# Optimization experiments

Hardware: AMD Instinct MI355X
Metric: run time of the kernel (lower is better)

The kernel has to match this reference:

```python
import jax, jax.numpy as jnp
import numpy as np

B, S, H, C = 8, 4096, 768, 64  # batch, seq_len, hidden_dim, block size


def _xavier(k, shape):
    fan = shape[0] + shape[1]
    return jax.random.normal(k, shape, jnp.float32) * np.sqrt(2.0 / fan)


def setup_inputs() -> dict:
    key = jax.random.key(0)
    kx, kq, kk, kv, k1, k2 = jax.random.split(key, 6)
    return {
        "x": jax.random.normal(kx, (B, S, H), jnp.float32),
        "Wq": _xavier(kq, (H, H)),
        "Wk": _xavier(kk, (H, H)),
        "Wv": _xavier(kv, (H, H)),
        "W1": _xavier(k1, (H, 16)),
        "W2": _xavier(k2, (16, H)),
        "b": jnp.zeros((H,), jnp.float32),
    }


def reference(x, Wq, Wk, Wv, W1, W2, b):
    Bb, Ss, Hh = x.shape
    NB = Ss // C  # number of blocks (seq_len divisible by C, no remainder)
    Q = x @ Wq
    K = x @ Wk
    V = x @ Wv
    # gating alpha: identical every block iteration in the original, compute once
    alpha = jax.nn.sigmoid((x @ W1) @ W2 + b) ** (1.0 / 16.0)  # [B,S,H]
    a = alpha.mean(axis=1, keepdims=True)  # [B,1,H], broadcasts over rows of state
    # blocks to leading axis for scan: [NB, B, C, H]
    qs = Q.reshape(Bb, NB, C, Hh).transpose(1, 0, 2, 3)
    ks = K.reshape(Bb, NB, C, Hh).transpose(1, 0, 2, 3)
    vs = V.reshape(Bb, NB, C, Hh).transpose(1, 0, 2, 3)
    mask = jnp.tril(jnp.ones((C, C), x.dtype))
    scale = 1.0 / np.sqrt(Hh).astype(np.float32)

    def step(St, blk):
        qb, kb, vb = blk  # each [B,C,H]
        # state update first (original updates S before computing output)
        St = St * a + jnp.einsum("bch,bcd->bhd", kb, vb)  # [B,H,H]
        # intra-block: scores masked by MULTIPLICATION (as in original), then softmax
        scores = jnp.einsum("bch,bdh->bcd", qb, kb) * mask * scale
        w = jax.nn.softmax(scores, axis=-1)
        out = jnp.einsum("bch,bhd->bcd", qb, St) + jnp.einsum("bcd,bde->bce", w, vb)
        return St, out

    S0 = jnp.zeros((Bb, Hh, Hh), x.dtype)
    _, outs = jax.lax.scan(step, S0, (qs, ks, vs))  # outs: [NB,B,C,H]
    O = outs.transpose(1, 0, 2, 3).reshape(Bb, Ss, Hh)
    return O
```

## Files before the change

kernel.cpp:

```cpp
#include <hip/hip_runtime.h>

#define B_ 8
#define S_ 4096
#define H_ 768
#define C_ 64
#define NB_ 64
#define M_ (B_*S_)

typedef _Float16 f16x8 __attribute__((ext_vector_type(8)));
typedef _Float16 f16x4 __attribute__((ext_vector_type(4)));
typedef float    f32x4 __attribute__((ext_vector_type(4)));

__global__ __launch_bounds__(256) void k_transpose(const float* __restrict__ src,
                                                   _Float16* __restrict__ dst) {
  __shared__ float tile[32][33];
  const int t = threadIdx.x;
  const int tx = t & 31, ty = t >> 5;
  const int n0 = blockIdx.x * 32, k0 = blockIdx.y * 32;
#pragma unroll
  for (int i = 0; i < 4; ++i)
    tile[ty + i*8][tx] = src[(k0 + ty + i*8) * H_ + n0 + tx];
  __syncthreads();
#pragma unroll
  for (int i = 0; i < 4; ++i)
    dst[(n0 + ty + i*8) * H_ + k0 + tx] = (_Float16)tile[tx][ty + i*8];
}

__global__ __launch_bounds__(256) void k_gemm_qkv(
    const float* __restrict__ x,
    const _Float16* __restrict__ WqT, const _Float16* __restrict__ WkT,
    const _Float16* __restrict__ WvT,
    _Float16* __restrict__ Qb, _Float16* __restrict__ Vb,
    _Float16* __restrict__ KT, _Float16* __restrict__ VT) {
  __shared__ _Float16 xs[64][40];
  __shared__ _Float16 ws[3][128][40];
  const int t = threadIdx.x;
  const int m0 = blockIdx.x * 64, n0 = blockIdx.y * 128;
  const int lane = t & 63, wv = t >> 6;
  const int lm = lane & 15, qd = lane >> 4;
  const int sm = t >> 2, sk = (t & 3) * 8;
  const int wn = t >> 1, wk = (t & 1) * 16;

  f32x4 acc[3][4][2];
#pragma unroll
  for (int a = 0; a < 3; ++a)
#pragma unroll
    for (int i = 0; i < 4; ++i)
#pragma unroll
      for (int n = 0; n < 2; ++n)
        acc[a][i][n] = (f32x4){0.f, 0.f, 0.f, 0.f};

  for (int kk = 0; kk < 24; ++kk) {
    const int k0 = kk * 32;
    __syncthreads();
    {
      const f32x4* xp = (const f32x4*)&x[(size_t)(m0 + sm) * H_ + k0 + sk];
      f32x4 f0 = xp[0], f1 = xp[1];
      f16x8 xv;
#pragma unroll
      for (int j = 0; j < 4; ++j) { xv[j] = (_Float16)f0[j]; xv[4 + j] = (_Float16)f1[j]; }
      *(f16x8*)&xs[sm][sk] = xv;
    }
    {
      const f16x8* wp = (const f16x8*)&WqT[(n0 + wn) * H_ + k0 + wk];
      *(f16x8*)&ws[0][wn][wk] = wp[0]; *(f16x8*)&ws[0][wn][wk + 8] = wp[1];
      wp = (const f16x8*)&WkT[(n0 + wn) * H_ + k0 + wk];
      *(f16x8*)&ws[1][wn][wk] = wp[0]; *(f16x8*)&ws[1][wn][wk + 8] = wp[1];
      wp = (const f16x8*)&WvT[(n0 + wn) * H_ + k0 + wk];
      *(f16x8*)&ws[2][wn][wk] = wp[0]; *(f16x8*)&ws[2][wn][wk + 8] = wp[1];
    }
    __syncthreads();
    f16x8 af[4];
#pragma unroll
    for (int i = 0; i < 4; ++i) af[i] = *(f16x8*)&xs[i*16 + lm][qd*8];
#pragma unroll
    for (int a = 0; a < 3; ++a)
#pragma unroll
      for (int n = 0; n < 2; ++n) {
        f16x8 bfr = *(f16x8*)&ws[a][wv*32 + n*16 + lm][qd*8];
#pragma unroll
        for (int i = 0; i < 4; ++i)
          acc[a][i][n] = __builtin_amdgcn_mfma_f32_16x16x32_f16(af[i], bfr, acc[a][i][n], 0, 0, 0);
      }
  }
#pragma unroll
  for (int i = 0; i < 4; ++i)
#pragma unroll
    for (int n = 0; n < 2; ++n) {
      const int ng = n0 + wv*32 + n*16 + lm;
      const int mg0 = m0 + i*16 + qd*4;
      const int bb = mg0 >> 12, ss = mg0 & (S_ - 1);
#pragma unroll
      for (int r = 0; r < 4; ++r) {
        Qb[(size_t)(mg0 + r) * H_ + ng] = (_Float16)acc[0][i][n][r];
        Vb[(size_t)(mg0 + r) * H_ + ng] = (_Float16)acc[2][i][n][r];
      }
      f16x4 kp, vp;
#pragma unroll
      for (int r = 0; r < 4; ++r) {
        kp[r] = (_Float16)acc[1][i][n][r];
        vp[r] = (_Float16)acc[2][i][n][r];
      }
      *(f16x4*)&KT[((size_t)bb * H_ + ng) * S_ + ss] = kp;
      *(f16x4*)&VT[((size_t)bb * H_ + ng) * S_ + ss] = vp;
    }
}

__global__ __launch_bounds__(256) void k_tgemm(const float* __restrict__ x,
                                               const float* __restrict__ W1,
                                               float* __restrict__ tbuf) {
  __shared__ float w1s[768 * 16];
  __shared__ float xs[64 * 129];
  const int t = threadIdx.x;
  const int m0 = blockIdx.x * 64;
  for (int i = t; i < 768 * 16 / 4; i += 256)
    ((f32x4*)w1s)[i] = ((const f32x4*)W1)[i];
  const int row = t & 63, cg = t >> 6;
  f32x4 acc = (f32x4){0.f, 0.f, 0.f, 0.f};
  for (int kc = 0; kc < 768; kc += 128) {
    __syncthreads();
    for (int i = 0; i < 32; ++i) {
      const int idx = t + 256 * i;
      const int r = idx >> 7, c = idx & 127;
      xs[r * 129 + c] = x[(size_t)(m0 + r) * H_ + kc + c];
    }
    __syncthreads();
#pragma unroll 8
    for (int kl = 0; kl < 128; ++kl) {
      const float a = xs[row * 129 + kl];
      const f32x4 w = *(const f32x4*)&w1s[(kc + kl) * 16 + cg * 4];
#pragma unroll
      for (int j = 0; j < 4; ++j) acc[j] += a * w[j];
    }
  }
  *(f32x4*)&tbuf[(size_t)(m0 + row) * 16 + cg * 4] = acc;
}

__global__ __launch_bounds__(256) void k_areduce(const float* __restrict__ tbuf,
                                                 const float* __restrict__ W2,
                                                 const float* __restrict__ bias,
                                                 float* __restrict__ abuf) {
  __shared__ float ts[128 * 17];
  __shared__ float rbuf[8 * 32];
  const int t = threadIdx.x;
  const int b = blockIdx.y, hc = blockIdx.x;
  const int hl = t & 31, sg = t >> 5;
  const int h = hc * 32 + hl;
  float w2r[16];
#pragma unroll
  for (int j = 0; j < 16; ++j) w2r[j] = W2[j * H_ + h];
  const float bb = bias[h];
  float asum = 0.f;
  const float* tb = &tbuf[(size_t)(b * S_) * 16];
  for (int sc = 0; sc < S_; sc += 128) {
    __syncthreads();
    for (int i = 0; i < 8; ++i) {
      const int idx = t + 256 * i;
      const int sl = idx >> 4, j = idx & 15;
      ts[sl * 17 + j] = tb[(size_t)(sc + sl) * 16 + j];
    }
    __syncthreads();
    for (int i = 0; i < 16; ++i) {
      const int sl = sg + i * 8;
      float z = bb;
      const float* tr = &ts[sl * 17];
#pragma unroll
      for (int j = 0; j < 16; ++j) z += tr[j] * w2r[j];
      const float sgm = 1.f / (1.f + __expf(-z));
      asum += sqrtf(sqrtf(sqrtf(sqrtf(sgm))));
    }
  }
  rbuf[sg * 32 + hl] = asum;
  __syncthreads();
  if (t < 32) {
    float s = 0.f;
#pragma unroll
    for (int g = 0; g < 8; ++g) s += rbuf[g * 32 + t];
    abuf[b * H_ + hc * 32 + t] = s * (1.f / (float)S_);
  }
}

__global__ __launch_bounds__(256) void k_scores_y(
    const _Float16* __restrict__ Qb, const _Float16* __restrict__ KT,
    const _Float16* __restrict__ Vb, float* __restrict__ O) {
  __shared__ float qs[64 * 68];
  __shared__ float ks[64 * 68];
  __shared__ float wb[64 * 68];
  __shared__ float vsb[64 * 68];
  const int t = threadIdx.x;
  const int nb = blockIdx.x, b = blockIdx.y;
  const size_t base = ((size_t)b * S_ + nb * 64) * H_;
  const int tc = t >> 4, td = t & 15;
  const int srow = t >> 2, sseg = (t & 3) * 16;

  float scr[4][4];
#pragma unroll
  for (int i = 0; i < 4; ++i)
#pragma unroll
    for (int u = 0; u < 4; ++u) scr[i][u] = 0.f;

  for (int hc = 0; hc < 12; ++hc) {
    __syncthreads();
    {
      const f16x8* qp = (const f16x8*)&Qb[base + (size_t)srow * H_ + hc * 64 + sseg];
      f16x8 q0 = qp[0], q1 = qp[1];
#pragma unroll
      for (int j = 0; j < 8; ++j) {
        qs[(sseg + j) * 68 + srow] = (float)q0[j];
        qs[(sseg + 8 + j) * 68 + srow] = (float)q1[j];
      }
    }
    {
      const size_t krow = ((size_t)b * H_ + hc * 64 + srow) * S_ + nb * 64 + sseg;
      f16x8 k0 = *(const f16x8*)&KT[krow];
      f16x8 k1 = *(const f16x8*)&KT[krow + 8];
      f32x4 f;
#pragma unroll
      for (int j = 0; j < 4; ++j) f[j] = (float)k0[j];
      *(f32x4*)&ks[srow * 68 + sseg] = f;
#pragma unroll
      for (int j = 0; j < 4; ++j) f[j] = (float)k0[4 + j];
      *(f32x4*)&ks[srow * 68 + sseg + 4] = f;
#pragma unroll
      for (int j = 0; j < 4; ++j) f[j] = (float)k1[j];
      *(f32x4*)&ks[srow * 68 + sseg + 8] = f;
#pragma unroll
      for (int j = 0; j < 4; ++j) f[j] = (float)k1[4 + j];
      *(f32x4*)&ks[srow * 68 + sseg + 12] = f;
    }
    __syncthreads();
#pragma unroll 4
    for (int h = 0; h < 64; ++h) {
      const f32x4 qv = *(f32x4*)&qs[h * 68 + tc * 4];
      const f32x4 kv = *(f32x4*)&ks[h * 68 + td * 4];
#pragma unroll
      for (int i = 0; i < 4; ++i)
#pragma unroll
        for (int u = 0; u < 4; ++u) scr[i][u] += qv[i] * kv[u];
    }
  }
  const float scale = 0.036084391824351615f;
#pragma unroll
  for (int i = 0; i < 4; ++i)
#pragma unroll
    for (int u = 0; u < 4; ++u) {
      const int c = tc * 4 + i, d = td * 4 + u;
      wb[d * 68 + c] = (d <= c) ? scr[i][u] * scale : 0.f;
    }
  __syncthreads();
  {
    const int r = t >> 2, g = t & 3;
    float vals[16];
    float mx = -1e30f;
#pragma unroll
    for (int i = 0; i < 16; ++i) {
      vals[i] = wb[(g * 16 + i) * 68 + r];
      mx = fmaxf(mx, vals[i]);
    }
    mx = fmaxf(mx, __shfl_xor(mx, 1));
    mx = fmaxf(mx, __shfl_xor(mx, 2));
    float sm = 0.f;
#pragma unroll
    for (int i = 0; i < 16; ++i) { vals[i] = __expf(vals[i] - mx); sm += vals[i]; }
    sm += __shfl_xor(sm, 1);
    sm += __shfl_xor(sm, 2);
    const float inv = 1.f / sm;
#pragma unroll
    for (int i = 0; i < 16; ++i) wb[(g * 16 + i) * 68 + r] = vals[i] * inv;
  }
  for (int ec = 0; ec < 12; ++ec) {
    __syncthreads();
    {
      const f16x8* vp = (const f16x8*)&Vb[base + (size_t)srow * H_ + ec * 64 + sseg];
      f16x8 v0 = vp[0], v1 = vp[1];
      f32x4 f;
#pragma unroll
      for (int j = 0; j < 4; ++j) f[j] = (float)v0[j];
      *(f32x4*)&vsb[srow * 68 + sseg] = f;
#pragma unroll
      for (int j = 0; j < 4; ++j) f[j] = (float)v0[4 + j];
      *(f32x4*)&vsb[srow * 68 + sseg + 4] = f;
#pragma unroll
      for (int j = 0; j < 4; ++j) f[j] = (float)v1[j];
      *(f32x4*)&vsb[srow * 68 + sseg + 8] = f;
#pragma unroll
      for (int j = 0; j < 4; ++j) f[j] = (float)v1[4 + j];
      *(f32x4*)&vsb[srow * 68 + sseg + 12] = f;
    }
    __syncthreads();
    float y[4][4];
#pragma unroll
    for (int i = 0; i < 4; ++i)
#pragma unroll
      for (int u = 0; u < 4; ++u) y[i][u] = 0.f;
#pragma unroll 4
    for (int j = 0; j < 64; ++j) {
      const f32x4 wv = *(f32x4*)&wb[j * 68 + tc * 4];
      const f32x4 vv = *(f32x4*)&vsb[j * 68 + td * 4];
#pragma unroll
      for (int i = 0; i < 4; ++i)
#pragma unroll
        for (int u = 0; u < 4; ++u) y[i][u] += wv[i] * vv[u];
    }
#pragma unroll
    for (int i = 0; i < 4; ++i) {
      f32x4 yv = {y[i][0], y[i][1], y[i][2], y[i][3]};
      *(f32x4*)&O[base + (size_t)(tc * 4 + i) * H_ + ec * 64 + td * 4] = yv;
    }
  }
}

#define STP 776
__global__ __launch_bounds__(256, 2) void k_scan(
    const _Float16* __restrict__ Qb, const _Float16* __restrict__ KT,
    const _Float16* __restrict__ VT, const float* __restrict__ abuf,
    float* __restrict__ O) {
  __shared__ _Float16 StL[32 * STP];
  const int t = threadIdx.x;
  const int b = blockIdx.y;
  const int d0 = blockIdx.x * 32;
  const int w = t >> 6, lane = t & 63;
  const int lm = lane & 15, qd = lane >> 4;

  const float av0 = abuf[b * H_ + d0 + lm];
  const float av1 = abuf[b * H_ + d0 + 16 + lm];

  f32x4 acc[12][2];
#pragma unroll
  for (int mt = 0; mt < 12; ++mt) {
    acc[mt][0] = (f32x4){0.f, 0.f, 0.f, 0.f};
    acc[mt][1] = (f32x4){0.f, 0.f, 0.f, 0.f};
  }

  const size_t ktb = (size_t)b * H_ * S_;
  const size_t vrow0 = ktb + (size_t)(d0 + lm) * S_;
  const size_t vrow1 = ktb + (size_t)(d0 + 16 + lm) * S_;

  for (int blk = 0; blk < NB_; ++blk) {
    const int s0 = blk * 64;
    f16x8 vf00 = *(const f16x8*)&VT[vrow0 + s0 + qd * 8];
    f16x8 vf01 = *(const f16x8*)&VT[vrow0 + s0 + 32 + qd * 8];
    f16x8 vf10 = *(const f16x8*)&VT[vrow1 + s0 + qd * 8];
    f16x8 vf11 = *(const f16x8*)&VT[vrow1 + s0 + 32 + qd * 8];
#pragma unroll
    for (int mt = 0; mt < 12; ++mt) {
      const size_t arow = ktb + (size_t)((w * 12 + mt) * 16 + lm) * S_ + s0 + qd * 8;
      f16x8 a0 = *(const f16x8*)&KT[arow];
      f16x8 a1 = *(const f16x8*)&KT[arow + 32];
      f32x4 c0 = acc[mt][0] * av0;
      f32x4 c1 = acc[mt][1] * av1;
      c0 = __builtin_amdgcn_mfma_f32_16x16x32_f16(a0, vf00, c0, 0, 0, 0);
      c0 = __builtin_amdgcn_mfma_f32_16x16x32_f16(a1, vf01, c0, 0, 0, 0);
      c1 = __builtin_amdgcn_mfma_f32_16x16x32_f16(a0, vf10, c1, 0, 0, 0);
      c1 = __builtin_amdgcn_mfma_f32_16x16x32_f16(a1, vf11, c1, 0, 0, 0);
      acc[mt][0] = c0;
      acc[mt][1] = c1;
    }
    __syncthreads();
#pragma unroll
    for (int mt = 0; mt < 12; ++mt) {
      const int h = (w * 12 + mt) * 16 + qd * 4;
      f16x4 p0, p1;
#pragma unroll
      for (int r = 0; r < 4; ++r) {
        p0[r] = (_Float16)acc[mt][0][r];
        p1[r] = (_Float16)acc[mt][1][r];
      }
      *(f16x4*)&StL[lm * STP + h] = p0;
      *(f16x4*)&StL[(16 + lm) * STP + h] = p1;
    }
    __syncthreads();
    f32x4 o0a = {0.f,0.f,0.f,0.f}, o0b = {0.f,0.f,0.f,0.f};
    f32x4 o1a = {0.f,0.f,0.f,0.f}, o1b = {0.f,0.f,0.f,0.f};
    const size_t qrow = ((size_t)b * S_ + s0 + w * 16 + lm) * H_ + qd * 8;
#pragma unroll 3
    for (int kt = 0; kt < 24; kt += 2) {
      f16x8 qa = *(const f16x8*)&Qb[qrow + kt * 32];
      f16x8 qb2 = *(const f16x8*)&Qb[qrow + kt * 32 + 32];
      f16x8 s00 = *(f16x8*)&StL[lm * STP + kt * 32 + qd * 8];
      f16x8 s01 = *(f16x8*)&StL[(16 + lm) * STP + kt * 32 + qd * 8];
      f16x8 s10 = *(f16x8*)&StL[lm * STP + kt * 32 + 32 + qd * 8];
      f16x8 s11 = *(f16x8*)&StL[(16 + lm) * STP + kt * 32 + 32 + qd * 8];
      o0a = __builtin_amdgcn_mfma_f32_16x16x32_f16(qa, s00, o0a, 0, 0, 0);
      o1a = __builtin_amdgcn_mfma_f32_16x16x32_f16(qa, s01, o1a, 0, 0, 0);
      o0b = __builtin_amdgcn_mfma_f32_16x16x32_f16(qb2, s10, o0b, 0, 0, 0);
      o1b = __builtin_amdgcn_mfma_f32_16x16x32_f16(qb2, s11, o1b, 0, 0, 0);
    }
    const f32x4 o0 = o0a + o0b;
    const f32x4 o1 = o1a + o1b;
    const size_t orow = ((size_t)b * S_ + s0 + w * 16 + qd * 4) * H_ + d0;
#pragma unroll
    for (int r = 0; r < 4; ++r) {
      O[orow + (size_t)r * H_ + lm] += o0[r];
      O[orow + (size_t)r * H_ + 16 + lm] += o1[r];
    }
  }
}

extern "C" void kernel_launch(void* const* d_in, const int* in_sizes, int n_in,
                              void* d_out, int out_size, void* d_ws, size_t ws_size,
                              hipStream_t stream) {
  (void)in_sizes; (void)n_in; (void)out_size; (void)ws_size;
  const float* x    = (const float*)d_in[0];
  const float* Wq   = (const float*)d_in[1];
  const float* Wk   = (const float*)d_in[2];
  const float* Wv   = (const float*)d_in[3];
  const float* W1   = (const float*)d_in[4];
  const float* W2   = (const float*)d_in[5];
  const float* bias = (const float*)d_in[6];
  float* O = (float*)d_out;

  char* ws = (char*)d_ws;
  _Float16* Qb  = (_Float16*)ws;
  _Float16* Vb  = Qb + (size_t)M_ * H_;
  _Float16* KT  = Vb + (size_t)M_ * H_;
  _Float16* VT  = KT + (size_t)M_ * H_;
  _Float16* WqT = VT + (size_t)M_ * H_;
  _Float16* WkT = WqT + H_ * H_;
  _Float16* WvT = WkT + H_ * H_;
  float* tbuf = (float*)(WvT + H_ * H_);
  float* abuf = tbuf + (size_t)M_ * 16;

  k_transpose<<<dim3(24, 24), 256, 0, stream>>>(Wq, WqT);
  k_transpose<<<dim3(24, 24), 256, 0, stream>>>(Wk, WkT);
  k_transpose<<<dim3(24, 24), 256, 0, stream>>>(Wv, WvT);
  k_gemm_qkv<<<dim3(512, 6), 256, 0, stream>>>(x, WqT, WkT, WvT, Qb, Vb, KT, VT);
  k_tgemm<<<dim3(512), 256, 0, stream>>>(x, W1, tbuf);
  k_areduce<<<dim3(24, 8), 256, 0, stream>>>(tbuf, W2, bias, abuf);
  k_scores_y<<<dim3(64, 8), 256, 0, stream>>>(Qb, KT, Vb, O);
  k_scan<<<dim3(24, 8), 256, 0, stream>>>(Qb, KT, VT, abuf, O);
}
```

Baseline: 1.536 ms.

## Split scan over hidden chunks with partial outputs, MFMA intra-block scores, prefetch K/V

The intra-block scores and softmax-weighted V product move from scalar fp32 LDS loops to MFMA fp16 instructions that read the transposed K and V buffers, so the row-major V buffer is dropped. The sequential scan kernel is split along the hidden (contraction) dimension into 2 or 4 chunks, picked by available workspace. This multiplies the number of blocks in the latency-bound scan, and K/V fragments for the next block are prefetched through register double-buffering. Each chunk writes fp16 partial outputs that a new reduce kernel adds into O. The cost is extra memory traffic for the partials and lower precision in the partial sums.

Result: slower. 1.876 ms (+22.1%).

```diff
diff --git a/kernel.cpp b/kernel.cpp
--- a/kernel.cpp
+++ b/kernel.cpp
@@ -30,8 +30,7 @@
     const float* __restrict__ x,
     const _Float16* __restrict__ WqT, const _Float16* __restrict__ WkT,
     const _Float16* __restrict__ WvT,
-    _Float16* __restrict__ Qb, _Float16* __restrict__ Vb,
-    _Float16* __restrict__ KT, _Float16* __restrict__ VT) {
+    _Float16* __restrict__ Qb, _Float16* __restrict__ KT, _Float16* __restrict__ VT) {
   __shared__ _Float16 xs[64][40];
   __shared__ _Float16 ws[3][128][40];
   const int t = threadIdx.x;
@@ -91,10 +90,8 @@
       const int mg0 = m0 + i*16 + qd*4;
       const int bb = mg0 >> 12, ss = mg0 & (S_ - 1);
 #pragma unroll
-      for (int r = 0; r < 4; ++r) {
+      for (int r = 0; r < 4; ++r)
         Qb[(size_t)(mg0 + r) * H_ + ng] = (_Float16)acc[0][i][n][r];
-        Vb[(size_t)(mg0 + r) * H_ + ng] = (_Float16)acc[2][i][n][r];
-      }
       f16x4 kp, vp;
 #pragma unroll
       for (int r = 0; r < 4; ++r) {
@@ -182,225 +179,224 @@
 
 __global__ __launch_bounds__(256) void k_scores_y(
     const _Float16* __restrict__ Qb, const _Float16* __restrict__ KT,
-    const _Float16* __restrict__ Vb, float* __restrict__ O) {
-  __shared__ float qs[64 * 68];
-  __shared__ float ks[64 * 68];
-  __shared__ float wb[64 * 68];
-  __shared__ float vsb[64 * 68];
+    const _Float16* __restrict__ VT, float* __restrict__ O) {
+  __shared__ _Float16 sbuf[64 * 136];
   const int t = threadIdx.x;
   const int nb = blockIdx.x, b = blockIdx.y;
-  const size_t base = ((size_t)b * S_ + nb * 64) * H_;
-  const int tc = t >> 4, td = t & 15;
-  const int srow = t >> 2, sseg = (t & 3) * 16;
-
-  float scr[4][4];
-#pragma unroll
-  for (int i = 0; i < 4; ++i)
-#pragma unroll
-    for (int u = 0; u < 4; ++u) scr[i][u] = 0.f;
-
-  for (int hc = 0; hc < 12; ++hc) {
+  const int s0 = nb * 64;
+  const int w = t >> 6, lane = t & 63;
+  const int lm = lane & 15, qd = lane >> 4;
+
+  f32x4 sc[4];
+#pragma unroll
+  for (int nt = 0; nt < 4; ++nt) sc[nt] = (f32x4){0.f, 0.f, 0.f, 0.f};
+
+  for (int hr = 0; hr < 6; ++hr) {
     __syncthreads();
     {
-      const f16x8* qp = (const f16x8*)&Qb[base + (size_t)srow * H_ + hc * 64 + sseg];
-      f16x8 q0 = qp[0], q1 = qp[1];
-#pragma unroll
-      for (int j = 0; j < 8; ++j) {
-        qs[(sseg + j) * 68 + srow] = (float)q0[j];
-        qs[(sseg + 8 + j) * 68 + srow] = (float)q1[j];
-      }
-    }
-    {
-      const size_t krow = ((size_t)b * H_ + hc * 64 + srow) * S_ + nb * 64 + sseg;
-      f16x8 k0 = *(const f16x8*)&KT[krow];
-      f16x8 k1 = *(const f16x8*)&KT[krow + 8];
-      f32x4 f;
-#pragma unroll
-      for (int j = 0; j < 4; ++j) f[j] = (float)k0[j];
-      *(f32x4*)&ks[srow * 68 + sseg] = f;
-#pragma unroll
-      for (int j = 0; j < 4; ++j) f[j] = (float)k0[4 + j];
-      *(f32x4*)&ks[srow * 68 + sseg + 4] = f;
-#pragma unroll
-      for (int j = 0; j < 4; ++j) f[j] = (float)k1[j];
-      *(f32x4*)&ks[srow * 68 + sseg + 8] = f;
-#pragma unroll
-      for (int j = 0; j < 4; ++j) f[j] = (float)k1[4 + j];
-      *(f32x4*)&ks[srow * 68 + sseg + 12] = f;
-    }
-    __syncthreads();
-#pragma unroll 4
-    for (int h = 0; h < 64; ++h) {
-      const f32x4 qv = *(f32x4*)&qs[h * 68 + tc * 4];
-      const f32x4 kv = *(f32x4*)&ks[h * 68 + td * 4];
-#pragma unroll
-      for (int i = 0; i < 4; ++i)
-#pragma unroll
-        for (int u = 0; u < 4; ++u) scr[i][u] += qv[i] * kv[u];
-    }
-  }
+      const int hl = t >> 1, dseg = (t & 1) * 32;
+      const size_t krow = ((size_t)b * H_ + hr * 128 + hl) * S_ + s0 + dseg;
+#pragma unroll
+      for (int j = 0; j < 4; ++j) {
+        f16x8 kv = *(const f16x8*)&KT[krow + j * 8];
+#pragma unroll
+        for (int u = 0; u < 8; ++u) sbuf[(dseg + j * 8 + u) * 136 + hl] = kv[u];
+      }
+    }
+    __syncthreads();
+    const size_t qrow = ((size_t)b * S_ + s0 + w * 16 + lm) * H_ + hr * 128 + qd * 8;
+#pragma unroll
+    for (int ktl = 0; ktl < 4; ++ktl) {
+      f16x8 qa = *(const f16x8*)&Qb[qrow + ktl * 32];
+#pragma unroll
+      for (int nt = 0; nt < 4; ++nt) {
+        f16x8 kb = *(f16x8*)&sbuf[(nt * 16 + lm) * 136 + ktl * 32 + qd * 8];
+        sc[nt] = __builtin_amdgcn_mfma_f32_16x16x32_f16(qa, kb, sc[nt], 0, 0, 0);
+      }
+    }
+  }
+  __syncthreads();
   const float scale = 0.036084391824351615f;
 #pragma unroll
-  for (int i = 0; i < 4; ++i)
-#pragma unroll
-    for (int u = 0; u < 4; ++u) {
-      const int c = tc * 4 + i, d = td * 4 + u;
-      wb[d * 68 + c] = (d <= c) ? scr[i][u] * scale : 0.f;
-    }
-  __syncthreads();
-  {
-    const int r = t >> 2, g = t & 3;
-    float vals[16];
-    float mx = -1e30f;
-#pragma unroll
-    for (int i = 0; i < 16; ++i) {
-      vals[i] = wb[(g * 16 + i) * 68 + r];
-      mx = fmaxf(mx, vals[i]);
+  for (int r = 0; r < 4; ++r) {
+    const int c = w * 16 + qd * 4 + r;
+    float v[4]; float mx = -1e30f;
+#pragma unroll
+    for (int nt = 0; nt < 4; ++nt) {
+      const int d = nt * 16 + lm;
+      v[nt] = (d <= c) ? sc[nt][r] * scale : 0.f;
+      mx = fmaxf(mx, v[nt]);
     }
     mx = fmaxf(mx, __shfl_xor(mx, 1));
     mx = fmaxf(mx, __shfl_xor(mx, 2));
+    mx = fmaxf(mx, __shfl_xor(mx, 4));
+    mx = fmaxf(mx, __shfl_xor(mx, 8));
     float sm = 0.f;
 #pragma unroll
-    for (int i = 0; i < 16; ++i) { vals[i] = __expf(vals[i] - mx); sm += vals[i]; }
+    for (int nt = 0; nt < 4; ++nt) { v[nt] = __expf(v[nt] - mx); sm += v[nt]; }
     sm += __shfl_xor(sm, 1);
     sm += __shfl_xor(sm, 2);
+    sm += __shfl_xor(sm, 4);
+    sm += __shfl_xor(sm, 8);
     const float inv = 1.f / sm;
 #pragma unroll
-    for (int i = 0; i < 16; ++i) wb[(g * 16 + i) * 68 + r] = vals[i] * inv;
-  }
-  for (int ec = 0; ec < 12; ++ec) {
-    __syncthreads();
-    {
-      const f16x8* vp = (const f16x8*)&Vb[base + (size_t)srow * H_ + ec * 64 + sseg];
-      f16x8 v0 = vp[0], v1 = vp[1];
-      f32x4 f;
-#pragma unroll
-      for (int j = 0; j < 4; ++j) f[j] = (float)v0[j];
-      *(f32x4*)&vsb[srow * 68 + sseg] = f;
-#pragma unroll
-      for (int j = 0; j < 4; ++j) f[j] = (float)v0[4 + j];
-      *(f32x4*)&vsb[srow * 68 + sseg + 4] = f;
-#pragma unroll
-      for (int j = 0; j < 4; ++j) f[j] = (float)v1[j];
-      *(f32x4*)&vsb[srow * 68 + sseg + 8] = f;
-#pragma unroll
-      for (int j = 0; j < 4; ++j) f[j] = (float)v1[4 + j];
-      *(f32x4*)&vsb[srow * 68 + sseg + 12] = f;
-    }
-    __syncthreads();
-    float y[4][4];
-#pragma unroll
-    for (int i = 0; i < 4; ++i)
-#pragma unroll
-      for (int u = 0; u < 4; ++u) y[i][u] = 0.f;
+    for (int nt = 0; nt < 4; ++nt)
+      sbuf[c * 72 + nt * 16 + lm] = (_Float16)(v[nt] * inv);
+  }
+  __syncthreads();
+  f16x8 wf[4][2];
+#pragma unroll
+  for (int nt = 0; nt < 4; ++nt)
+#pragma unroll
+    for (int kd = 0; kd < 2; ++kd)
+      wf[nt][kd] = *(f16x8*)&sbuf[(nt * 16 + lm) * 72 + kd * 32 + qd * 8];
 #pragma unroll 4
-    for (int j = 0; j < 64; ++j) {
-      const f32x4 wv = *(f32x4*)&wb[j * 68 + tc * 4];
-      const f32x4 vv = *(f32x4*)&vsb[j * 68 + td * 4];
-#pragma unroll
-      for (int i = 0; i < 4; ++i)
-#pragma unroll
-        for (int u = 0; u < 4; ++u) y[i][u] += wv[i] * vv[u];
-    }
-#pragma unroll
-    for (int i = 0; i < 4; ++i) {
-      f32x4 yv = {y[i][0], y[i][1], y[i][2], y[i][3]};
-      *(f32x4*)&O[base + (size_t)(tc * 4 + i) * H_ + ec * 64 + td * 4] = yv;
-    }
-  }
-}
-
-#define STP 776
-__global__ __launch_bounds__(256, 2) void k_scan(
+  for (int mt = 0; mt < 12; ++mt) {
+    const int e0 = (w * 12 + mt) * 16;
+    const size_t ar = ((size_t)b * H_ + e0 + lm) * S_ + s0 + qd * 8;
+    f16x8 a0 = *(const f16x8*)&VT[ar];
+    f16x8 a1 = *(const f16x8*)&VT[ar + 32];
+#pragma unroll
+    for (int nt = 0; nt < 4; ++nt) {
+      f32x4 y = (f32x4){0.f, 0.f, 0.f, 0.f};
+      y = __builtin_amdgcn_mfma_f32_16x16x32_f16(a0, wf[nt][0], y, 0, 0, 0);
+      y = __builtin_amdgcn_mfma_f32_16x16x32_f16(a1, wf[nt][1], y, 0, 0, 0);
+      *(f32x4*)&O[((size_t)b * S_ + s0 + nt * 16 + lm) * H_ + e0 + qd * 4] = y;
+    }
+  }
+}
+
+template<int HC>
+__global__ __launch_bounds__(256, (HC == 4 ? 3 : 2)) void k_scan(
     const _Float16* __restrict__ Qb, const _Float16* __restrict__ KT,
     const _Float16* __restrict__ VT, const float* __restrict__ abuf,
-    float* __restrict__ O) {
+    _Float16* __restrict__ P, size_t pstride) {
+  constexpr int HCH = H_ / HC;
+  constexpr int MT  = HCH / 64;
+  constexpr int KT2 = HCH / 32;
+  constexpr int STP = HCH + 8;
   __shared__ _Float16 StL[32 * STP];
   const int t = threadIdx.x;
-  const int b = blockIdx.y;
   const int d0 = blockIdx.x * 32;
+  const int hcb = blockIdx.y;
+  const int b = blockIdx.z;
   const int w = t >> 6, lane = t & 63;
   const int lm = lane & 15, qd = lane >> 4;
 
   const float av0 = abuf[b * H_ + d0 + lm];
   const float av1 = abuf[b * H_ + d0 + 16 + lm];
 
-  f32x4 acc[12][2];
-#pragma unroll
-  for (int mt = 0; mt < 12; ++mt) {
+  f32x4 acc[MT][2];
+#pragma unroll
+  for (int mt = 0; mt < MT; ++mt) {
     acc[mt][0] = (f32x4){0.f, 0.f, 0.f, 0.f};
     acc[mt][1] = (f32x4){0.f, 0.f, 0.f, 0.f};
   }
 
-  const size_t ktb = (size_t)b * H_ * S_;
-  const size_t vrow0 = ktb + (size_t)(d0 + lm) * S_;
-  const size_t vrow1 = ktb + (size_t)(d0 + 16 + lm) * S_;
-
+  const size_t ktbase = (size_t)b * H_;
+  const size_t krow = (ktbase + hcb * HCH + w * MT * 16 + lm) * S_ + qd * 8;
+  const size_t vrow0 = (ktbase + d0 + lm) * S_ + qd * 8;
+  const size_t vrow1 = (ktbase + d0 + 16 + lm) * S_ + qd * 8;
+
+  f16x8 kfb[2][MT][2];
+  f16x8 vfb[2][2][2];
+#pragma unroll
+  for (int mt = 0; mt < MT; ++mt) {
+    kfb[0][mt][0] = *(const f16x8*)&KT[krow + (size_t)mt * 16 * S_];
+    kfb[0][mt][1] = *(const f16x8*)&KT[krow + (size_t)mt * 16 * S_ + 32];
+  }
+  vfb[0][0][0] = *(const f16x8*)&VT[vrow0];
+  vfb[0][0][1] = *(const f16x8*)&VT[vrow0 + 32];
+  vfb[0][1][0] = *(const f16x8*)&VT[vrow1];
+  vfb[0][1][1] = *(const f16x8*)&VT[vrow1 + 32];
+
+  _Float16* Pp = P + (size_t)hcb * pstride;
+
+#pragma unroll 1
   for (int blk = 0; blk < NB_; ++blk) {
+    const int cur = blk & 1, nxt = cur ^ 1;
     const int s0 = blk * 64;
-    f16x8 vf00 = *(const f16x8*)&VT[vrow0 + s0 + qd * 8];
-    f16x8 vf01 = *(const f16x8*)&VT[vrow0 + s0 + 32 + qd * 8];
-    f16x8 vf10 = *(const f16x8*)&VT[vrow1 + s0 + qd * 8];
-    f16x8 vf11 = *(const f16x8*)&VT[vrow1 + s0 + 32 + qd * 8];
-#pragma unroll
-    for (int mt = 0; mt < 12; ++mt) {
-      const size_t arow = ktb + (size_t)((w * 12 + mt) * 16 + lm) * S_ + s0 + qd * 8;
-      f16x8 a0 = *(const f16x8*)&KT[arow];
-      f16x8 a1 = *(const f16x8*)&KT[arow + 32];
+    f16x8 qf[KT2];
+    const size_t qrow = ((size_t)b * S_ + s0 + w * 16 + lm) * H_ + hcb * HCH + qd * 8;
+#pragma unroll
+    for (int kt = 0; kt < KT2; ++kt) qf[kt] = *(const f16x8*)&Qb[qrow + kt * 32];
+#pragma unroll
+    for (int mt = 0; mt < MT; ++mt) {
       f32x4 c0 = acc[mt][0] * av0;
       f32x4 c1 = acc[mt][1] * av1;
-      c0 = __builtin_amdgcn_mfma_f32_16x16x32_f16(a0, vf00, c0, 0, 0, 0);
-      c0 = __builtin_amdgcn_mfma_f32_16x16x32_f16(a1, vf01, c0, 0, 0, 0);
-      c1 = __builtin_amdgcn_mfma_f32_16x16x32_f16(a0, vf10, c1, 0, 0, 0);
-      c1 = __builtin_amdgcn_mfma_f32_16x16x32_f16(a1, vf11, c1, 0, 0, 0);
+      c0 = __builtin_amdgcn_mfma_f32_16x16x32_f16(kfb[cur][mt][0], vfb[cur][0][0], c0, 0, 0, 0);
+      c0 = __builtin_amdgcn_mfma_f32_16x16x32_f16(kfb[cur][mt][1], vfb[cur][0][1], c0, 0, 0, 0);
+      c1 = __builtin_amdgcn_mfma_f32_16x16x32_f16(kfb[cur][mt][0], vfb[cur][1][0], c1, 0, 0, 0);
+      c1 = __builtin_amdgcn_mfma_f32_16x16x32_f16(kfb[cur][mt][1], vfb[cur][1][1], c1, 0, 0, 0);
       acc[mt][0] = c0;
       acc[mt][1] = c1;
     }
     __syncthreads();
 #pragma unroll
-    for (int mt = 0; mt < 12; ++mt) {
-      const int h = (w * 12 + mt) * 16 + qd * 4;
+    for (int mt = 0; mt < MT; ++mt) {
+      const int hl = (w * MT + mt) * 16 + qd * 4;
       f16x4 p0, p1;
 #pragma unroll
       for (int r = 0; r < 4; ++r) {
         p0[r] = (_Float16)acc[mt][0][r];
         p1[r] = (_Float16)acc[mt][1][r];
       }
-      *(f16x4*)&StL[lm * STP + h] = p0;
-      *(f16x4*)&StL[(16 + lm) * STP + h] = p1;
-    }
-    __syncthreads();
-    f32x4 o0a = {0.f,0.f,0.f,0.f}, o0b = {0.f,0.f,0.f,0.f};
-    f32x4 o1a = {0.f,0.f,0.f,0.f}, o1b = {0.f,0.f,0.f,0.f};
-    const size_t qrow = ((size_t)b * S_ + s0 + w * 16 + lm) * H_ + qd * 8;
-#pragma unroll 3
-    for (int kt = 0; kt < 24; kt += 2) {
-      f16x8 qa = *(const f16x8*)&Qb[qrow + kt * 32];
-      f16x8 qb2 = *(const f16x8*)&Qb[qrow + kt * 32 + 32];
-      f16x8 s00 = *(f16x8*)&StL[lm * STP + kt * 32 + qd * 8];
-      f16x8 s01 = *(f16x8*)&StL[(16 + lm) * STP + kt * 32 + qd * 8];
-      f16x8 s10 = *(f16x8*)&StL[lm * STP + kt * 32 + 32 + qd * 8];
-      f16x8 s11 = *(f16x8*)&StL[(16 + lm) * STP + kt * 32 + 32 + qd * 8];
-      o0a = __builtin_amdgcn_mfma_f32_16x16x32_f16(qa, s00, o0a, 0, 0, 0);
-      o1a = __builtin_amdgcn_mfma_f32_16x16x32_f16(qa, s01, o1a, 0, 0, 0);
-      o0b = __builtin_amdgcn_mfma_f32_16x16x32_f16(qb2, s10, o0b, 0, 0, 0);
-      o1b = __builtin_amdgcn_mfma_f32_16x16x32_f16(qb2, s11, o1b, 0, 0, 0);
-    }
-    const f32x4 o0 = o0a + o0b;
-    const f32x4 o1 = o1a + o1b;
-    const size_t orow = ((size_t)b * S_ + s0 + w * 16 + qd * 4) * H_ + d0;
-#pragma unroll
-    for (int r = 0; r < 4; ++r) {
-      O[orow + (size_t)r * H_ + lm] += o0[r];
-      O[orow + (size_t)r * H_ + 16 + lm] += o1[r];
-    }
+      *(f16x4*)&StL[lm * STP + hl] = p0;
+      *(f16x4*)&StL[(16 + lm) * STP + hl] = p1;
+    }
+    __syncthreads();
+    if (blk < NB_ - 1) {
+      const int s1 = s0 + 64;
+#pragma unroll
+      for (int mt = 0; mt < MT; ++mt) {
+        kfb[nxt][mt][0] = *(const f16x8*)&KT[krow + (size_t)mt * 16 * S_ + s1];
+        kfb[nxt][mt][1] = *(const f16x8*)&KT[krow + (size_t)mt * 16 * S_ + s1 + 32];
+      }
+      vfb[nxt][0][0] = *(const f16x8*)&VT[vrow0 + s1];
+      vfb[nxt][0][1] = *(const f16x8*)&VT[vrow0 + s1 + 32];
+      vfb[nxt][1][0] = *(const f16x8*)&VT[vrow1 + s1];
+      vfb[nxt][1][1] = *(const f16x8*)&VT[vrow1 + s1 + 32];
+    }
+    f32x4 o0 = (f32x4){0.f, 0.f, 0.f, 0.f};
+    f32x4 o1 = (f32x4){0.f, 0.f, 0.f, 0.f};
+#pragma unroll
+    for (int kt = 0; kt < KT2; ++kt) {
+      f16x8 a0 = *(f16x8*)&StL[lm * STP + kt * 32 + qd * 8];
+      f16x8 a1 = *(f16x8*)&StL[(16 + lm) * STP + kt * 32 + qd * 8];
+      o0 = __builtin_amdgcn_mfma_f32_16x16x32_f16(a0, qf[kt], o0, 0, 0, 0);
+      o1 = __builtin_amdgcn_mfma_f32_16x16x32_f16(a1, qf[kt], o1, 0, 0, 0);
+    }
+    const size_t prow = ((size_t)b * S_ + s0 + w * 16 + lm) * H_ + d0 + qd * 4;
+    f16x4 q0, q1;
+#pragma unroll
+    for (int r = 0; r < 4; ++r) { q0[r] = (_Float16)o0[r]; q1[r] = (_Float16)o1[r]; }
+    *(f16x4*)&Pp[prow] = q0;
+    *(f16x4*)&Pp[prow + 16] = q1;
+  }
+}
+
+template<int HC>
+__global__ __launch_bounds__(256) void k_reduce(const _Float16* __restrict__ P,
+                                                size_t pstride, float* __restrict__ O) {
+  const int total = M_ * H_ / 8;
+  for (int i = blockIdx.x * 256 + threadIdx.x; i < total; i += gridDim.x * 256) {
+    f32x4 o0 = ((f32x4*)O)[i * 2];
+    f32x4 o1 = ((f32x4*)O)[i * 2 + 1];
+#pragma unroll
+    for (int hc = 0; hc < HC; ++hc) {
+      f16x8 p = ((const f16x8*)(P + hc * pstride))[i];
+#pragma unroll
+      for (int j = 0; j < 4; ++j) { o0[j] += (float)p[j]; o1[j] += (float)p[4 + j]; }
+    }
+    ((f32x4*)O)[i * 2] = o0;
+    ((f32x4*)O)[i * 2 + 1] = o1;
   }
 }
 
 extern "C" void kernel_launch(void* const* d_in, const int* in_sizes, int n_in,
                               void* d_out, int out_size, void* d_ws, size_t ws_size,
                               hipStream_t stream) {
-  (void)in_sizes; (void)n_in; (void)out_size; (void)ws_size;
+  (void)in_sizes; (void)n_in; (void)out_size;
   const float* x    = (const float*)d_in[0];
   const float* Wq   = (const float*)d_in[1];
   const float* Wk   = (const float*)d_in[2];
@@ -410,23 +406,33 @@
   const float* bias = (const float*)d_in[6];
   float* O = (float*)d_out;
 
+  const size_t nQKV = (size_t)M_ * H_;
   char* ws = (char*)d_ws;
   _Float16* Qb  = (_Float16*)ws;
-  _Float16* Vb  = Qb + (size_t)M_ * H_;
-  _Float16* KT  = Vb + (size_t)M_ * H_;
-  _Float16* VT  = KT + (size_t)M_ * H_;
-  _Float16* WqT = VT + (size_t)M_ * H_;
+  _Float16* KT  = Qb + nQKV;
+  _Float16* VT  = KT + nQKV;
+  _Float16* WqT = VT + nQKV;
   _Float16* WkT = WqT + H_ * H_;
   _Float16* WvT = WkT + H_ * H_;
   float* tbuf = (float*)(WvT + H_ * H_);
   float* abuf = tbuf + (size_t)M_ * 16;
+  _Float16* P = (_Float16*)(abuf + B_ * H_);
+
+  const size_t base = (size_t)((char*)P - ws);
+  const bool hc4 = ws_size >= base + 4 * nQKV * sizeof(_Float16);
 
   k_transpose<<<dim3(24, 24), 256, 0, stream>>>(Wq, WqT);
   k_transpose<<<dim3(24, 24), 256, 0, stream>>>(Wk, WkT);
   k_transpose<<<dim3(24, 24), 256, 0, stream>>>(Wv, WvT);
-  k_gemm_qkv<<<dim3(512, 6), 256, 0, stream>>>(x, WqT, WkT, WvT, Qb, Vb, KT, VT);
+  k_gemm_qkv<<<dim3(512, 6), 256, 0, stream>>>(x, WqT, WkT, WvT, Qb, KT, VT);
   k_tgemm<<<dim3(512), 256, 0, stream>>>(x, W1, tbuf);
   k_areduce<<<dim3(24, 8), 256, 0, stream>>>(tbuf, W2, bias, abuf);
-  k_scores_y<<<dim3(64, 8), 256, 0, stream>>>(Qb, KT, Vb, O);
-  k_scan<<<dim3(24, 8), 256, 0, stream>>>(Qb, KT, VT, abuf, O);
-}
+  k_scores_y<<<dim3(64, 8), 256, 0, stream>>>(Qb, KT, VT, O);
+  if (hc4) {
+    k_scan<4><<<dim3(24, 4, 8), 256, 0, stream>>>(Qb, KT, VT, abuf, P, nQKV);
+    k_reduce<4><<<dim3(4096), 256, 0, stream>>>(P, nQKV, O);
+  } else {
+    k_scan<2><<<dim3(24, 2, 8), 256, 0, stream>>>(Qb, KT, VT, abuf, P, nQKV);
+    k_reduce<2><<<dim3(4096), 256, 0, stream>>>(P, nQKV, O);
+  }
+}
```
